# Kernel optimization log

Hardware: AMD Instinct MI355X
Metric: run time of the kernel (lower is better)

The kernel has to match this reference:

```python
import jax, jax.numpy as jnp
import numpy as np

V, D, H, F, L, B, S = 32000, 1024, 16, 4096, 6, 2, 1024
DH = D // H


def setup_inputs() -> dict:
    key = jax.random.key(0)
    ks = jax.random.split(key, 12)
    n = lambda k, shape: jax.random.normal(k, shape, jnp.float32) * 0.02
    inp = {}
    inp['x'] = jax.random.randint(ks[0], (B, S), 0, V)
    # causal mask: 1 = masked (upper triangle), matches masked_fill(mask==1, -inf)
    inp['mask'] = jnp.triu(jnp.ones((S, S), jnp.int32), k=1)[None, None]
    inp['embed'] = n(ks[1], (V, D))
    inp['wq'] = n(ks[2], (L, D, D)); inp['bq'] = jnp.zeros((L, D), jnp.float32)
    inp['wk'] = n(ks[3], (L, D, D)); inp['bk'] = jnp.zeros((L, D), jnp.float32)
    inp['wv'] = n(ks[4], (L, D, D)); inp['bv'] = jnp.zeros((L, D), jnp.float32)
    inp['wo'] = n(ks[5], (L, D, D)); inp['bo'] = jnp.zeros((L, D), jnp.float32)
    inp['w1'] = n(ks[6], (L, D, F)); inp['b1'] = jnp.zeros((L, F), jnp.float32)
    inp['w2'] = n(ks[7], (L, F, D)); inp['b2'] = jnp.zeros((L, D), jnp.float32)
    inp['ln1_g'] = jnp.ones((L, D), jnp.float32); inp['ln1_b'] = jnp.zeros((L, D), jnp.float32)
    inp['ln2_g'] = jnp.ones((L, D), jnp.float32); inp['ln2_b'] = jnp.zeros((L, D), jnp.float32)
    inp['lnf_g'] = jnp.ones((D,), jnp.float32); inp['lnf_b'] = jnp.zeros((D,), jnp.float32)
    inp['proj_w'] = n(ks[8], (D, V)); inp['proj_b'] = jnp.zeros((V,), jnp.float32)
    return inp


def _layernorm(x, g, b, eps=1e-5):
    mu = jnp.mean(x, axis=-1, keepdims=True)
    var = jnp.var(x, axis=-1, keepdims=True)
    return (x - mu) * jax.lax.rsqrt(var + eps) * g + b


def _positional_encoding(s, d):
    pos = jnp.arange(s, dtype=jnp.float32)[:, None]
    div = jnp.exp(jnp.arange(0, d, 2, dtype=jnp.float32) * (-jnp.log(10000.0) / d))
    pe = jnp.zeros((s, d), jnp.float32)
    pe = pe.at[:, 0::2].set(jnp.sin(pos * div))
    pe = pe.at[:, 1::2].set(jnp.cos(pos * div))
    return pe


def reference(x, mask, embed, wq, bq, wk, bk, wv, bv, wo, bo, w1, b1, w2, b2,
              ln1_g, ln1_b, ln2_g, ln2_b, lnf_g, lnf_b, proj_w, proj_b):
    b_, s_ = x.shape
    h = embed[x] * jnp.sqrt(jnp.float32(D))          # [B,S,D]
    h = h + _positional_encoding(s_, D)[None]
    scale = 1.0 / jnp.sqrt(jnp.float32(DH))

    def layer(h, p):
        Wq, Bq, Wk, Bk, Wv, Bv, Wo, Bo, W1, B1, W2, B2, G1, Be1, G2, Be2 = p
        q = (h @ Wq + Bq).reshape(b_, s_, H, DH).transpose(0, 2, 1, 3)   # [B,H,S,Dh]
        k = (h @ Wk + Bk).reshape(b_, s_, H, DH).transpose(0, 2, 1, 3)
        v = (h @ Wv + Bv).reshape(b_, s_, H, DH).transpose(0, 2, 1, 3)
        scores = jnp.einsum('bhqd,bhkd->bhqk', q, k) * scale            # [B,H,S,S]
        scores = jnp.where(mask == 1, -jnp.inf, scores)
        attn = jax.nn.softmax(scores, axis=-1)
        ctx = jnp.einsum('bhqk,bhkd->bhqd', attn, v)
        ctx = ctx.transpose(0, 2, 1, 3).reshape(b_, s_, D) @ Wo + Bo
        h = _layernorm(h + ctx, G1, Be1)
        ffn = jax.nn.relu(h @ W1 + B1) @ W2 + B2
        h = _layernorm(h + ffn, G2, Be2)
        return h, None

    h, _ = jax.lax.scan(layer, h, (wq, bq, wk, bk, wv, bv, wo, bo,
                                   w1, b1, w2, b2, ln1_g, ln1_b, ln2_g, ln2_b))
    h = _layernorm(h, lnf_g, lnf_b)
    return h @ proj_w + proj_b                                           # [B,S,V]
```

## Files before the change

### kernel.cpp

```cpp
#include <hip/hip_runtime.h>
#include <math.h>

#define D_MODEL 1024
#define NHEADS 16
#define DHEAD 64
#define FDIM 4096
#define NLAYERS 6
#define BATCH 2
#define SEQ 1024
#define NROWS (BATCH*SEQ)
#define VOCAB 32000

typedef __attribute__((ext_vector_type(4))) float f32x4;
typedef __attribute__((ext_vector_type(4))) __bf16 bf16x4;
typedef __attribute__((ext_vector_type(8))) __bf16 bf16x8;

__device__ __forceinline__ void gll16(const void* g, void* l) {
  __builtin_amdgcn_global_load_lds(
      (const __attribute__((address_space(1))) unsigned int*)g,
      (__attribute__((address_space(3))) unsigned int*)l, 16, 0, 0);
}

__global__ __launch_bounds__(256) void transpose_w(
    const float* __restrict__ W, __bf16* __restrict__ Wt, int K, int N) {
  __shared__ __bf16 Ls[64][68];
  const size_t moff = (size_t)blockIdx.z * K * N;
  const float* Wl = W + moff;
  __bf16* Wtl = Wt + moff;
  const int n0 = blockIdx.x * 64, k0 = blockIdx.y * 64;
  const int tid = threadIdx.x;
  #pragma unroll
  for (int p = 0; p < 4; ++p) {
    int e = tid + p * 256;
    int r = e >> 4, c4 = (e & 15) * 4;
    float4 v = *(const float4*)&Wl[(size_t)(k0 + r) * N + n0 + c4];
    Ls[c4 + 0][r] = (__bf16)v.x; Ls[c4 + 1][r] = (__bf16)v.y;
    Ls[c4 + 2][r] = (__bf16)v.z; Ls[c4 + 3][r] = (__bf16)v.w;
  }
  __syncthreads();
  #pragma unroll
  for (int p = 0; p < 4; ++p) {
    int e = tid + p * 256;
    int r2 = e >> 4, c8 = (e & 15) * 4;
    bf16x4 o{Ls[r2][c8], Ls[r2][c8 + 1], Ls[r2][c8 + 2], Ls[r2][c8 + 3]};
    *(bf16x4*)&Wtl[(size_t)(n0 + r2) * K + k0 + c8] = o;
  }
}

struct GemmP {
  const __bf16* A;
  const __bf16* W[3];
  const float* B[3];
  void* C[3];
  int N, K;
};

template<int BM, int RELU, int OUTF32>
__global__ __launch_bounds__(256) void gemm_bf16(GemmP g) {
  constexpr int BK = 64;
  const __bf16* __restrict__ A = g.A;
  const __bf16* __restrict__ W = g.W[blockIdx.z];
  const float* __restrict__ bias = g.B[blockIdx.z];
  const int N = g.N, K = g.K;

  __shared__ __bf16 As[2][BM * BK];
  __shared__ __bf16 Bs[2][128 * BK];

  const int tid = threadIdx.x;
  const int lane = tid & 63, w = tid >> 6;

  const int gx = gridDim.x;
  const int nblk = gx * gridDim.y;
  const int id = blockIdx.x + blockIdx.y * gx;
  const int per = nblk >> 3;
  const int sid = (id & 7) * per + (id >> 3);
  const int row0 = (sid % gx) * BM;
  const int col0 = (sid / gx) * 128;

  const int wm = w >> 1, wn = w & 1;
  const int lr = lane & 15, rsw = lr & 7;

  constexpr int MI = BM / 32;
  f32x4 acc[MI][4] = {};

  const int swg = ((lane & 7) ^ (lane >> 3)) * 8;
  const __bf16* Ag = A + (size_t)(row0 + w * (BM / 4) + (lane >> 3)) * K + swg;
  const __bf16* Wg = W + (size_t)(col0 + w * 32 + (lane >> 3)) * K + swg;

  const int NT = K / BK;

  auto stage = [&](int buf, int t) {
    const int k0 = t * BK;
    #pragma unroll
    for (int s = 0; s < BM / 32; ++s)
      gll16(Ag + (size_t)s * 8 * K + k0, &As[buf][(w * (BM / 4) + s * 8) * BK]);
    #pragma unroll
    for (int s = 0; s < 4; ++s)
      gll16(Wg + (size_t)s * 8 * K + k0, &Bs[buf][(w * 32 + s * 8) * BK]);
  };

  stage(0, 0);
  __syncthreads();

  int cur = 0;
  for (int t = 0; t < NT; ++t) {
    if (t + 1 < NT) stage(cur ^ 1, t + 1);
    #pragma unroll
    for (int kk = 0; kk < 2; ++kk) {
      const int gsw = ((kk * 4 + (lane >> 4)) ^ rsw) * 8;
      bf16x8 af[MI], bf[4];
      #pragma unroll
      for (int i = 0; i < MI; ++i)
        af[i] = *(const bf16x8*)&As[cur][(wm * (BM / 2) + i * 16 + lr) * BK + gsw];
      #pragma unroll
      for (int j = 0; j < 4; ++j)
        bf[j] = *(const bf16x8*)&Bs[cur][(wn * 64 + j * 16 + lr) * BK + gsw];
      #pragma unroll
      for (int i = 0; i < MI; ++i)
        #pragma unroll
        for (int j = 0; j < 4; ++j)
          acc[i][j] = __builtin_amdgcn_mfma_f32_16x16x32_bf16(af[i], bf[j], acc[i][j], 0, 0, 0);
    }
    __syncthreads();
    cur ^= 1;
  }

  #pragma unroll
  for (int i = 0; i < MI; ++i) {
    #pragma unroll
    for (int j = 0; j < 4; ++j) {
      int col = col0 + wn * 64 + j * 16 + lr;
      float bb = bias[col];
      #pragma unroll
      for (int r = 0; r < 4; ++r) {
        int row = row0 + wm * (BM / 2) + i * 16 + (lane >> 4) * 4 + r;
        float v = acc[i][j][r] + bb;
        if (RELU) v = fmaxf(v, 0.0f);
        if (OUTF32) ((float*)g.C[blockIdx.z])[(size_t)row * N + col] = v;
        else ((__bf16*)g.C[blockIdx.z])[(size_t)row * N + col] = (__bf16)v;
      }
    }
  }
}

__global__ __launch_bounds__(512, 2) void gemm_256(
    const __bf16* __restrict__ A, const __bf16* __restrict__ W,
    const float* __restrict__ bias, float* __restrict__ C, int N, int K) {
  extern __shared__ __bf16 sm[];
  __bf16* Asm = sm;
  __bf16* Bsm = sm + 2 * 256 * 64;

  const int tid = threadIdx.x;
  const int lane = tid & 63, w = tid >> 6;

  const int gx = gridDim.x;
  const int nblk = gx * gridDim.y;
  const int id = blockIdx.x + blockIdx.y * gx;
  const int per = nblk >> 3;
  const int sid = (id & 7) * per + (id >> 3);
  const int row0 = (sid % gx) * 256;
  const int col0 = (sid / gx) * 256;

  const int wr = w >> 2, wc = w & 3;
  const int lr = lane & 15;

  f32x4 acc[8][4] = {};

  const int swg = ((lane & 7) ^ (lane >> 3)) * 8;
  const __bf16* Agb = A + (size_t)(row0 + (lane >> 3)) * K + swg;
  const __bf16* Wgb = W + (size_t)(col0 + (lane >> 3)) * K + swg;

  const int NT = K / 64;

  auto stage_half = [&](int idx) {
    const int tile = idx >> 2, half = idx & 3;
    const int buf = tile & 1;
    const int k0 = tile * 64;
    const int rowbase = (half & 1) * 128 + w * 16;
    const __bf16* src = (half < 2 ? Wgb : Agb) + (size_t)rowbase * K + k0;
    __bf16* dst = (half < 2 ? Bsm : Asm) + buf * 16384 + rowbase * 64;
    gll16(src, dst);
    gll16(src + (size_t)8 * K, dst + 8 * 64);
  };

  #pragma unroll
  for (int i = 0; i < 5; ++i) stage_half(i);
  asm volatile("s_waitcnt vmcnt(2)" ::: "memory");
  __builtin_amdgcn_s_barrier();

  for (int t = 0; t < NT; ++t) {
    const int cur = t & 1;
    bf16x8 bfr[4][2];
    #pragma unroll
    for (int h = 0; h < 4; ++h) {
      if (h == 0) {
        #pragma unroll
        for (int j = 0; j < 4; ++j) {
          int row = wc * 64 + j * 16 + lr;
          #pragma unroll
          for (int kk = 0; kk < 2; ++kk)
            bfr[j][kk] = *(const bf16x8*)&Bsm[cur * 16384 + row * 64 +
                                              (((kk * 4 + (lane >> 4)) ^ (row & 7)) * 8)];
        }
      }
      bf16x8 afr[2][2];
      #pragma unroll
      for (int ii = 0; ii < 2; ++ii) {
        int row = wr * 128 + (2 * h + ii) * 16 + lr;
        #pragma unroll
        for (int kk = 0; kk < 2; ++kk)
          afr[ii][kk] = *(const bf16x8*)&Asm[cur * 16384 + row * 64 +
                                             (((kk * 4 + (lane >> 4)) ^ (row & 7)) * 8)];
      }
      const int sidx = 4 * t + h + 5;
      if (sidx < 4 * NT) stage_half(sidx);
      if (h == 3) {
        if (t + 2 < NT) asm volatile("s_waitcnt vmcnt(2)" ::: "memory");
        else if (t + 1 < NT) asm volatile("s_waitcnt vmcnt(0)" ::: "memory");
      }
      __builtin_amdgcn_s_barrier();
      __builtin_amdgcn_s_setprio(1);
      #pragma unroll
      for (int kk = 0; kk < 2; ++kk)
        #pragma unroll
        for (int ii = 0; ii < 2; ++ii)
          #pragma unroll
          for (int j = 0; j < 4; ++j)
            acc[2 * h + ii][j] = __builtin_amdgcn_mfma_f32_16x16x32_bf16(
                afr[ii][kk], bfr[j][kk], acc[2 * h + ii][j], 0, 0, 0);
      __builtin_amdgcn_s_setprio(0);
      __builtin_amdgcn_s_barrier();
    }
  }

  #pragma unroll
  for (int i = 0; i < 8; ++i) {
    #pragma unroll
    for (int j = 0; j < 4; ++j) {
      int col = col0 + wc * 64 + j * 16 + lr;
      float bb = bias[col];
      #pragma unroll
      for (int r = 0; r < 4; ++r) {
        int row = row0 + wr * 128 + i * 16 + (lane >> 4) * 4 + r;
        C[(size_t)row * N + col] = acc[i][j][r] + bb;
      }
    }
  }
}

__global__ __launch_bounds__(256) void attn_kernel(
    const __bf16* __restrict__ Q, const __bf16* __restrict__ K,
    const __bf16* __restrict__ V, __bf16* __restrict__ O) {
  __shared__ __bf16 Ks[64 * 64];
  __shared__ __bf16 Vts[64 * 64];
  __shared__ __bf16 Psm[4][16 * 64];

  const int tid = threadIdx.x;
  const int lane = tid & 63, w = tid >> 6;
  const int q0 = blockIdx.x * 64;
  const int bh = blockIdx.y;
  const int b = bh >> 4, h = bh & 15;
  const size_t base = ((size_t)b * SEQ) * D_MODEL + (size_t)h * DHEAD;

  const int lr = lane & 15;
  const int lk = (lane >> 4) * 8;

  bf16x8 qa[2];
  {
    const __bf16* qp = Q + base + (size_t)(q0 + w * 16 + lr) * D_MODEL;
    qa[0] = *(const bf16x8*)&qp[lk];
    qa[1] = *(const bf16x8*)&qp[32 + lk];
  }

  f32x4 o_acc[4] = {};
  float m[4], l[4];
  #pragma unroll
  for (int r = 0; r < 4; ++r) { m[r] = -1e30f; l[r] = 0.0f; }

  const int nck = q0 / 64 + 1;

  for (int ck = 0; ck < nck; ++ck) {
    const int kv0 = ck * 64;
    __syncthreads();
    #pragma unroll
    for (int c = 0; c < 2; ++c) {
      int e = tid + c * 256;
      int r = e >> 3, d8 = (e & 7) * 8;
      const size_t grow = base + (size_t)(kv0 + r) * D_MODEL + d8;
      bf16x8 kv = *(const bf16x8*)&K[grow];
      *(bf16x8*)&Ks[(r * 64 + d8) ^ ((r & 7) << 3)] = kv;
      bf16x8 vv = *(const bf16x8*)&V[grow];
      #pragma unroll
      for (int j = 0; j < 8; ++j)
        Vts[((d8 + j) * 64 + r) ^ (((d8 + j) & 7) << 3)] = vv[j];
    }
    __syncthreads();

    f32x4 s_acc[4] = {};
    #pragma unroll
    for (int t = 0; t < 4; ++t) {
      int row = t * 16 + lr;
      #pragma unroll
      for (int hh = 0; hh < 2; ++hh) {
        bf16x8 kb = *(const bf16x8*)&Ks[(row * 64 + hh * 32 + lk) ^ ((row & 7) << 3)];
        s_acc[t] = __builtin_amdgcn_mfma_f32_16x16x32_bf16(qa[hh], kb, s_acc[t], 0, 0, 0);
      }
    }

    const bool diag = (ck == nck - 1);
    #pragma unroll
    for (int t = 0; t < 4; ++t) {
      int kvg = kv0 + t * 16 + lr;
      #pragma unroll
      for (int r = 0; r < 4; ++r) {
        float sv = s_acc[t][r] * 0.125f;
        if (diag) {
          int qg = q0 + w * 16 + (lane >> 4) * 4 + r;
          if (kvg > qg) sv = -1e30f;
        }
        s_acc[t][r] = sv;
      }
    }

    #pragma unroll
    for (int r = 0; r < 4; ++r) {
      float cm = fmaxf(fmaxf(s_acc[0][r], s_acc[1][r]), fmaxf(s_acc[2][r], s_acc[3][r]));
      #pragma unroll
      for (int off = 1; off < 16; off <<= 1) cm = fmaxf(cm, __shfl_xor(cm, off, 64));
      float newm = fmaxf(m[r], cm);
      float sc = __expf(m[r] - newm);
      m[r] = newm;
      float psum = 0.0f;
      #pragma unroll
      for (int t = 0; t < 4; ++t) {
        float p = __expf(s_acc[t][r] - newm);
        s_acc[t][r] = p;
        psum += p;
      }
      #pragma unroll
      for (int off = 1; off < 16; off <<= 1) psum += __shfl_xor(psum, off, 64);
      l[r] = l[r] * sc + psum;
      #pragma unroll
      for (int t = 0; t < 4; ++t) o_acc[t][r] *= sc;
    }

    #pragma unroll
    for (int t = 0; t < 4; ++t) {
      #pragma unroll
      for (int r = 0; r < 4; ++r) {
        int ql = (lane >> 4) * 4 + r;
        Psm[w][(ql * 64 + t * 16 + lr) ^ ((ql & 7) << 3)] = (__bf16)(s_acc[t][r]);
      }
    }

    bf16x8 pa[2];
    #pragma unroll
    for (int hh = 0; hh < 2; ++hh)
      pa[hh] = *(const bf16x8*)&Psm[w][(lr * 64 + hh * 32 + lk) ^ ((lr & 7) << 3)];
    #pragma unroll
    for (int t = 0; t < 4; ++t) {
      int row = t * 16 + lr;
      #pragma unroll
      for (int hh = 0; hh < 2; ++hh) {
        bf16x8 vb = *(const bf16x8*)&Vts[(row * 64 + hh * 32 + lk) ^ ((row & 7) << 3)];
        o_acc[t] = __builtin_amdgcn_mfma_f32_16x16x32_bf16(pa[hh], vb, o_acc[t], 0, 0, 0);
      }
    }
  }

  #pragma unroll
  for (int r = 0; r < 4; ++r) {
    float inv = 1.0f / l[r];
    int qg = q0 + w * 16 + (lane >> 4) * 4 + r;
    #pragma unroll
    for (int t = 0; t < 4; ++t)
      O[base + (size_t)qg * D_MODEL + t * 16 + lr] = (__bf16)(o_acc[t][r] * inv);
  }
}

template<int HASRES>
__global__ __launch_bounds__(256) void addln_kernel(
    const __bf16* __restrict__ X, const __bf16* __restrict__ Rr,
    const float* __restrict__ g, const float* __restrict__ bb,
    __bf16* __restrict__ Out) {
  const int row = blockIdx.x;
  const int tid = threadIdx.x;
  const size_t rb = (size_t)row * D_MODEL + tid * 4;
  bf16x4 xv = *(const bf16x4*)&X[rb];
  float v[4];
  float s = 0.0f, ss = 0.0f;
  if (HASRES) {
    bf16x4 rv = *(const bf16x4*)&Rr[rb];
    #pragma unroll
    for (int i = 0; i < 4; ++i) {
      v[i] = (float)xv[i] + (float)rv[i];
      s += v[i]; ss += v[i] * v[i];
    }
  } else {
    #pragma unroll
    for (int i = 0; i < 4; ++i) { v[i] = (float)xv[i]; s += v[i]; ss += v[i] * v[i]; }
  }
  #pragma unroll
  for (int off = 32; off; off >>= 1) { s += __shfl_xor(s, off, 64); ss += __shfl_xor(ss, off, 64); }
  __shared__ float red[8];
  const int lane = tid & 63, w = tid >> 6;
  if (lane == 0) { red[w] = s; red[4 + w] = ss; }
  __syncthreads();
  s = red[0] + red[1] + red[2] + red[3];
  ss = red[4] + red[5] + red[6] + red[7];
  float mean = s * (1.0f / D_MODEL);
  float var = ss * (1.0f / D_MODEL) - mean * mean;
  float rs = rsqrtf(var + 1e-5f);
  const int d0 = tid * 4;
  bf16x4 ov;
  #pragma unroll
  for (int i = 0; i < 4; ++i)
    ov[i] = (__bf16)((v[i] - mean) * rs * g[d0 + i] + bb[d0 + i]);
  *(bf16x4*)&Out[rb] = ov;
}

__global__ __launch_bounds__(256) void embed_kernel(
    const int* __restrict__ x, const float* __restrict__ embed,
    __bf16* __restrict__ H) {
  const int row = blockIdx.x;
  const int spos = row & (SEQ - 1);
  const int tok = x[row];
  const int tid = threadIdx.x;
  const int d0 = tid * 4;
  float4 e4 = *(const float4*)&embed[(size_t)tok * D_MODEL + d0];
  float ev[4] = {e4.x, e4.y, e4.z, e4.w};
  bf16x4 ov;
  #pragma unroll
  for (int i = 0; i < 4; ++i) {
    int d = d0 + i;
    float div = expf((float)(2 * (d >> 1)) * (-9.2103403719761836f / (float)D_MODEL));
    float ang = (float)spos * div;
    float pe = (d & 1) ? cosf(ang) : sinf(ang);
    ov[i] = (__bf16)(ev[i] * 32.0f + pe);
  }
  *(bf16x4*)&H[(size_t)row * D_MODEL + d0] = ov;
}

extern "C" void kernel_launch(void* const* d_in, const int* in_sizes, int n_in,
                              void* d_out, int out_size, void* d_ws, size_t ws_size,
                              hipStream_t stream) {
  const int* x = (const int*)d_in[0];
  const float* embed = (const float*)d_in[2];
  const float* wq = (const float*)d_in[3];
  const float* bq = (const float*)d_in[4];
  const float* wk = (const float*)d_in[5];
  const float* bk = (const float*)d_in[6];
  const float* wv = (const float*)d_in[7];
  const float* bv = (const float*)d_in[8];
  const float* wo = (const float*)d_in[9];
  const float* bo = (const float*)d_in[10];
  const float* w1 = (const float*)d_in[11];
  const float* b1 = (const float*)d_in[12];
  const float* w2 = (const float*)d_in[13];
  const float* b2 = (const float*)d_in[14];
  const float* ln1g = (const float*)d_in[15];
  const float* ln1b = (const float*)d_in[16];
  const float* ln2g = (const float*)d_in[17];
  const float* ln2b = (const float*)d_in[18];
  const float* lnfg = (const float*)d_in[19];
  const float* lnfb = (const float*)d_in[20];
  const float* pw = (const float*)d_in[21];
  const float* pb = (const float*)d_in[22];
  float* out = (float*)d_out;

  char* wsp = (char*)d_ws;
  size_t off = 0;
  auto alloc = [&](size_t bytes) {
    void* p = wsp + off; off = (off + bytes + 255) & ~(size_t)255; return p;
  };
  const size_t RD2 = (size_t)NROWS * D_MODEL * 2;
  __bf16* Xb   = (__bf16*)alloc(RD2);
  __bf16* Qb   = (__bf16*)alloc(RD2);
  __bf16* Kb   = (__bf16*)alloc(RD2);
  __bf16* Vb   = (__bf16*)alloc(RD2);
  __bf16* CTXb = (__bf16*)alloc(RD2);
  __bf16* Tb   = (__bf16*)alloc(RD2);
  __bf16* H1b  = (__bf16*)alloc(RD2);
  __bf16* FFb  = Qb;
  const size_t DD = (size_t)D_MODEL * D_MODEL;
  const size_t DF = (size_t)D_MODEL * FDIM;
  __bf16* wqt = (__bf16*)alloc(NLAYERS * DD * 2);
  __bf16* wkt = (__bf16*)alloc(NLAYERS * DD * 2);
  __bf16* wvt = (__bf16*)alloc(NLAYERS * DD * 2);
  __bf16* wot = (__bf16*)alloc(NLAYERS * DD * 2);
  __bf16* w1t = (__bf16*)alloc(NLAYERS * DF * 2);
  __bf16* w2t = (__bf16*)alloc(NLAYERS * DF * 2);
  __bf16* pwt = (__bf16*)alloc((size_t)D_MODEL * VOCAB * 2);

  transpose_w<<<dim3(16, 16, NLAYERS), 256, 0, stream>>>(wq, wqt, D_MODEL, D_MODEL);
  transpose_w<<<dim3(16, 16, NLAYERS), 256, 0, stream>>>(wk, wkt, D_MODEL, D_MODEL);
  transpose_w<<<dim3(16, 16, NLAYERS), 256, 0, stream>>>(wv, wvt, D_MODEL, D_MODEL);
  transpose_w<<<dim3(16, 16, NLAYERS), 256, 0, stream>>>(wo, wot, D_MODEL, D_MODEL);
  transpose_w<<<dim3(64, 16, NLAYERS), 256, 0, stream>>>(w1, w1t, D_MODEL, FDIM);
  transpose_w<<<dim3(16, 64, NLAYERS), 256, 0, stream>>>(w2, w2t, FDIM, D_MODEL);
  transpose_w<<<dim3(500, 16, 1), 256, 0, stream>>>(pw, pwt, D_MODEL, VOCAB);

  embed_kernel<<<NROWS, 256, 0, stream>>>(x, embed, Xb);

  for (int l = 0; l < NLAYERS; ++l) {
    GemmP g{};
    g.A = Xb; g.N = D_MODEL; g.K = D_MODEL;
    g.W[0] = wqt + l * DD; g.W[1] = wkt + l * DD; g.W[2] = wvt + l * DD;
    g.B[0] = bq + l * D_MODEL; g.B[1] = bk + l * D_MODEL; g.B[2] = bv + l * D_MODEL;
    g.C[0] = Qb; g.C[1] = Kb; g.C[2] = Vb;
    gemm_bf16<128, 0, 0><<<dim3(NROWS / 128, D_MODEL / 128, 3), 256, 0, stream>>>(g);

    attn_kernel<<<dim3(SEQ / 64, BATCH * NHEADS), 256, 0, stream>>>(Qb, Kb, Vb, CTXb);

    GemmP go{};
    go.A = CTXb; go.N = D_MODEL; go.K = D_MODEL;
    go.W[0] = wot + l * DD; go.B[0] = bo + l * D_MODEL; go.C[0] = Tb;
    gemm_bf16<64, 0, 0><<<dim3(NROWS / 64, D_MODEL / 128, 1), 256, 0, stream>>>(go);

    addln_kernel<1><<<NROWS, 256, 0, stream>>>(Xb, Tb, ln1g + l * D_MODEL, ln1b + l * D_MODEL, H1b);

    GemmP g1{};
    g1.A = H1b; g1.N = FDIM; g1.K = D_MODEL;
    g1.W[0] = w1t + l * DF; g1.B[0] = b1 + l * FDIM; g1.C[0] = FFb;
    gemm_bf16<128, 1, 0><<<dim3(NROWS / 128, FDIM / 128, 1), 256, 0, stream>>>(g1);

    GemmP g2{};
    g2.A = FFb; g2.N = D_MODEL; g2.K = FDIM;
    g2.W[0] = w2t + l * DF; g2.B[0] = b2 + l * D_MODEL; g2.C[0] = Tb;
    gemm_bf16<64, 0, 0><<<dim3(NROWS / 64, D_MODEL / 128, 1), 256, 0, stream>>>(g2);

    addln_kernel<1><<<NROWS, 256, 0, stream>>>(H1b, Tb, ln2g + l * D_MODEL, ln2b + l * D_MODEL, Xb);
  }

  addln_kernel<0><<<NROWS, 256, 0, stream>>>(Xb, nullptr, lnfg, lnfb, H1b);

  hipFuncSetAttribute((const void*)gemm_256,
                      hipFuncAttributeMaxDynamicSharedMemorySize, 131072);
  gemm_256<<<dim3(NROWS / 256, VOCAB / 256), 512, 131072, stream>>>(
      H1b, pwt, pb, out, VOCAB, D_MODEL);
}
```

Measured before the change: 1.510 ms.

## Fuse QKV weights into one wide GEMM and widen attention blocks to 128 queries

Packs the transposed Q, K and V weights into a single 3072-wide matrix so the projection runs as one GEMM with BM=64 and an interleaved QKV output buffer, picking the bias by column. The attention kernel now reads directly from the interleaved buffer with a 3072 stride and processes 128 queries per block with 512 threads, so each K/V tile loaded into shared memory is shared by twice as many query rows. The causal mask is now applied on every chunk instead of only the diagonal one, which adds some compare work. Fewer, larger attention blocks also lower the block count, which may leave some compute units idle.

```diff
diff --git a/kernel.cpp b/kernel.cpp
--- a/kernel.cpp
+++ b/kernel.cpp
@@ -22,11 +22,11 @@
 }
 
 __global__ __launch_bounds__(256) void transpose_w(
-    const float* __restrict__ W, __bf16* __restrict__ Wt, int K, int N) {
+    const float* __restrict__ W, __bf16* __restrict__ Wt, int K, int N,
+    size_t out_lstride, int row_off) {
   __shared__ __bf16 Ls[64][68];
-  const size_t moff = (size_t)blockIdx.z * K * N;
-  const float* Wl = W + moff;
-  __bf16* Wtl = Wt + moff;
+  const float* Wl = W + (size_t)blockIdx.z * K * N;
+  __bf16* Wtl = Wt + (size_t)blockIdx.z * out_lstride + (size_t)row_off * K;
   const int n0 = blockIdx.x * 64, k0 = blockIdx.y * 64;
   const int tid = threadIdx.x;
   #pragma unroll
@@ -55,12 +55,11 @@
   int N, K;
 };
 
-template<int BM, int RELU, int OUTF32>
+template<int BM, int RELU, int OUTF32, int MULTIBIAS>
 __global__ __launch_bounds__(256) void gemm_bf16(GemmP g) {
   constexpr int BK = 64;
   const __bf16* __restrict__ A = g.A;
   const __bf16* __restrict__ W = g.W[blockIdx.z];
-  const float* __restrict__ bias = g.B[blockIdx.z];
   const int N = g.N, K = g.K;
 
   __shared__ __bf16 As[2][BM * BK];
@@ -130,7 +129,7 @@
     #pragma unroll
     for (int j = 0; j < 4; ++j) {
       int col = col0 + wn * 64 + j * 16 + lr;
-      float bb = bias[col];
+      float bb = MULTIBIAS ? g.B[col >> 10][col & 1023] : g.B[blockIdx.z][col];
       #pragma unroll
       for (int r = 0; r < 4; ++r) {
         int row = row0 + wm * (BM / 2) + i * 16 + (lane >> 4) * 4 + r;
@@ -248,26 +247,26 @@
   }
 }
 
-__global__ __launch_bounds__(256) void attn_kernel(
-    const __bf16* __restrict__ Q, const __bf16* __restrict__ K,
-    const __bf16* __restrict__ V, __bf16* __restrict__ O) {
+__global__ __launch_bounds__(512) void attn_kernel(
+    const __bf16* __restrict__ QKV, __bf16* __restrict__ O) {
   __shared__ __bf16 Ks[64 * 64];
   __shared__ __bf16 Vts[64 * 64];
-  __shared__ __bf16 Psm[4][16 * 64];
+  __shared__ __bf16 Psm[8][16 * 64];
 
   const int tid = threadIdx.x;
   const int lane = tid & 63, w = tid >> 6;
-  const int q0 = blockIdx.x * 64;
+  const int q0 = blockIdx.x * 128;
   const int bh = blockIdx.y;
   const int b = bh >> 4, h = bh & 15;
-  const size_t base = ((size_t)b * SEQ) * D_MODEL + (size_t)h * DHEAD;
+  const size_t qb = ((size_t)b * SEQ) * 3072 + (size_t)h * DHEAD;
+  const size_t ob = ((size_t)b * SEQ) * D_MODEL + (size_t)h * DHEAD;
 
   const int lr = lane & 15;
   const int lk = (lane >> 4) * 8;
 
   bf16x8 qa[2];
   {
-    const __bf16* qp = Q + base + (size_t)(q0 + w * 16 + lr) * D_MODEL;
+    const __bf16* qp = QKV + qb + (size_t)(q0 + w * 16 + lr) * 3072;
     qa[0] = *(const bf16x8*)&qp[lk];
     qa[1] = *(const bf16x8*)&qp[32 + lk];
   }
@@ -277,19 +276,17 @@
   #pragma unroll
   for (int r = 0; r < 4; ++r) { m[r] = -1e30f; l[r] = 0.0f; }
 
-  const int nck = q0 / 64 + 1;
+  const int nck = q0 / 64 + 2;
 
   for (int ck = 0; ck < nck; ++ck) {
     const int kv0 = ck * 64;
     __syncthreads();
-    #pragma unroll
-    for (int c = 0; c < 2; ++c) {
-      int e = tid + c * 256;
-      int r = e >> 3, d8 = (e & 7) * 8;
-      const size_t grow = base + (size_t)(kv0 + r) * D_MODEL + d8;
-      bf16x8 kv = *(const bf16x8*)&K[grow];
+    {
+      int r = tid >> 3, d8 = (tid & 7) * 8;
+      const size_t grow = qb + (size_t)(kv0 + r) * 3072 + d8;
+      bf16x8 kv = *(const bf16x8*)&QKV[grow + 1024];
       *(bf16x8*)&Ks[(r * 64 + d8) ^ ((r & 7) << 3)] = kv;
-      bf16x8 vv = *(const bf16x8*)&V[grow];
+      bf16x8 vv = *(const bf16x8*)&QKV[grow + 2048];
       #pragma unroll
       for (int j = 0; j < 8; ++j)
         Vts[((d8 + j) * 64 + r) ^ (((d8 + j) & 7) << 3)] = vv[j];
@@ -307,17 +304,14 @@
       }
     }
 
-    const bool diag = (ck == nck - 1);
     #pragma unroll
     for (int t = 0; t < 4; ++t) {
       int kvg = kv0 + t * 16 + lr;
       #pragma unroll
       for (int r = 0; r < 4; ++r) {
         float sv = s_acc[t][r] * 0.125f;
-        if (diag) {
-          int qg = q0 + w * 16 + (lane >> 4) * 4 + r;
-          if (kvg > qg) sv = -1e30f;
-        }
+        int qg = q0 + w * 16 + (lane >> 4) * 4 + r;
+        if (kvg > qg) sv = -1e30f;
         s_acc[t][r] = sv;
       }
     }
@@ -374,7 +368,7 @@
     int qg = q0 + w * 16 + (lane >> 4) * 4 + r;
     #pragma unroll
     for (int t = 0; t < 4; ++t)
-      O[base + (size_t)qg * D_MODEL + t * 16 + lr] = (__bf16)(o_acc[t][r] * inv);
+      O[ob + (size_t)qg * D_MODEL + t * 16 + lr] = (__bf16)(o_acc[t][r] * inv);
   }
 }
 
@@ -475,59 +469,56 @@
   };
   const size_t RD2 = (size_t)NROWS * D_MODEL * 2;
   __bf16* Xb   = (__bf16*)alloc(RD2);
-  __bf16* Qb   = (__bf16*)alloc(RD2);
-  __bf16* Kb   = (__bf16*)alloc(RD2);
-  __bf16* Vb   = (__bf16*)alloc(RD2);
+  __bf16* QKVb = (__bf16*)alloc((size_t)NROWS * 3072 * 2);
   __bf16* CTXb = (__bf16*)alloc(RD2);
   __bf16* Tb   = (__bf16*)alloc(RD2);
   __bf16* H1b  = (__bf16*)alloc(RD2);
-  __bf16* FFb  = Qb;
+  __bf16* FFb  = QKVb;
   const size_t DD = (size_t)D_MODEL * D_MODEL;
   const size_t DF = (size_t)D_MODEL * FDIM;
-  __bf16* wqt = (__bf16*)alloc(NLAYERS * DD * 2);
-  __bf16* wkt = (__bf16*)alloc(NLAYERS * DD * 2);
-  __bf16* wvt = (__bf16*)alloc(NLAYERS * DD * 2);
+  const size_t D3 = (size_t)3072 * D_MODEL;
+  __bf16* wqkvt = (__bf16*)alloc(NLAYERS * D3 * 2);
   __bf16* wot = (__bf16*)alloc(NLAYERS * DD * 2);
   __bf16* w1t = (__bf16*)alloc(NLAYERS * DF * 2);
   __bf16* w2t = (__bf16*)alloc(NLAYERS * DF * 2);
   __bf16* pwt = (__bf16*)alloc((size_t)D_MODEL * VOCAB * 2);
 
-  transpose_w<<<dim3(16, 16, NLAYERS), 256, 0, stream>>>(wq, wqt, D_MODEL, D_MODEL);
-  transpose_w<<<dim3(16, 16, NLAYERS), 256, 0, stream>>>(wk, wkt, D_MODEL, D_MODEL);
-  transpose_w<<<dim3(16, 16, NLAYERS), 256, 0, stream>>>(wv, wvt, D_MODEL, D_MODEL);
-  transpose_w<<<dim3(16, 16, NLAYERS), 256, 0, stream>>>(wo, wot, D_MODEL, D_MODEL);
-  transpose_w<<<dim3(64, 16, NLAYERS), 256, 0, stream>>>(w1, w1t, D_MODEL, FDIM);
-  transpose_w<<<dim3(16, 64, NLAYERS), 256, 0, stream>>>(w2, w2t, FDIM, D_MODEL);
-  transpose_w<<<dim3(500, 16, 1), 256, 0, stream>>>(pw, pwt, D_MODEL, VOCAB);
+  transpose_w<<<dim3(16, 16, NLAYERS), 256, 0, stream>>>(wq, wqkvt, D_MODEL, D_MODEL, D3, 0);
+  transpose_w<<<dim3(16, 16, NLAYERS), 256, 0, stream>>>(wk, wqkvt, D_MODEL, D_MODEL, D3, 1024);
+  transpose_w<<<dim3(16, 16, NLAYERS), 256, 0, stream>>>(wv, wqkvt, D_MODEL, D_MODEL, D3, 2048);
+  transpose_w<<<dim3(16, 16, NLAYERS), 256, 0, stream>>>(wo, wot, D_MODEL, D_MODEL, DD, 0);
+  transpose_w<<<dim3(64, 16, NLAYERS), 256, 0, stream>>>(w1, w1t, D_MODEL, FDIM, DF, 0);
+  transpose_w<<<dim3(16, 64, NLAYERS), 256, 0, stream>>>(w2, w2t, FDIM, D_MODEL, DF, 0);
+  transpose_w<<<dim3(500, 16, 1), 256, 0, stream>>>(pw, pwt, D_MODEL, VOCAB, (size_t)D_MODEL * VOCAB, 0);
 
   embed_kernel<<<NROWS, 256, 0, stream>>>(x, embed, Xb);
 
   for (int l = 0; l < NLAYERS; ++l) {
     GemmP g{};
-    g.A = Xb; g.N = D_MODEL; g.K = D_MODEL;
-    g.W[0] = wqt + l * DD; g.W[1] = wkt + l * DD; g.W[2] = wvt + l * DD;
+    g.A = Xb; g.N = 3072; g.K = D_MODEL;
+    g.W[0] = wqkvt + l * D3;
     g.B[0] = bq + l * D_MODEL; g.B[1] = bk + l * D_MODEL; g.B[2] = bv + l * D_MODEL;
-    g.C[0] = Qb; g.C[1] = Kb; g.C[2] = Vb;
-    gemm_bf16<128, 0, 0><<<dim3(NROWS / 128, D_MODEL / 128, 3), 256, 0, stream>>>(g);
-
-    attn_kernel<<<dim3(SEQ / 64, BATCH * NHEADS), 256, 0, stream>>>(Qb, Kb, Vb, CTXb);
+    g.C[0] = QKVb;
+    gemm_bf16<64, 0, 0, 1><<<dim3(NROWS / 64, 3072 / 128, 1), 256, 0, stream>>>(g);
+
+    attn_kernel<<<dim3(SEQ / 128, BATCH * NHEADS), 512, 0, stream>>>(QKVb, CTXb);
 
     GemmP go{};
     go.A = CTXb; go.N = D_MODEL; go.K = D_MODEL;
     go.W[0] = wot + l * DD; go.B[0] = bo + l * D_MODEL; go.C[0] = Tb;
-    gemm_bf16<64, 0, 0><<<dim3(NROWS / 64, D_MODEL / 128, 1), 256, 0, stream>>>(go);
+    gemm_bf16<64, 0, 0, 0><<<dim3(NROWS / 64, D_MODEL / 128, 1), 256, 0, stream>>>(go);
 
     addln_kernel<1><<<NROWS, 256, 0, stream>>>(Xb, Tb, ln1g + l * D_MODEL, ln1b + l * D_MODEL, H1b);
 
     GemmP g1{};
     g1.A = H1b; g1.N = FDIM; g1.K = D_MODEL;
     g1.W[0] = w1t + l * DF; g1.B[0] = b1 + l * FDIM; g1.C[0] = FFb;
-    gemm_bf16<128, 1, 0><<<dim3(NROWS / 128, FDIM / 128, 1), 256, 0, stream>>>(g1);
+    gemm_bf16<128, 1, 0, 0><<<dim3(NROWS / 128, FDIM / 128, 1), 256, 0, stream>>>(g1);
 
     GemmP g2{};
     g2.A = FFb; g2.N = D_MODEL; g2.K = FDIM;
     g2.W[0] = w2t + l * DF; g2.B[0] = b2 + l * D_MODEL; g2.C[0] = Tb;
-    gemm_bf16<64, 0, 0><<<dim3(NROWS / 64, D_MODEL / 128, 1), 256, 0, stream>>>(g2);
+    gemm_bf16<64, 0, 0, 0><<<dim3(NROWS / 64, D_MODEL / 128, 1), 256, 0, stream>>>(g2);
 
     addln_kernel<1><<<NROWS, 256, 0, stream>>>(H1b, Tb, ln2g + l * D_MODEL, ln2b + l * D_MODEL, Xb);
   }
```

Result: no change. 1.520 ms (+0.6%).
